# Performance work log

Measured on AMD Instinct MI355X. Metric: run time of the kernel, lower is better.

The kernel has to match this reference:

```python
import jax, jax.numpy as jnp
import numpy as np

# Dimensions (all layers are mLSTM due to the constructor bug: `if w` tests the
# whole truthy `which` list, so signature=(2,1) still yields 3 mLSTM layers).
L, S, B, I = 3, 512, 4, 512      # layers, seq_len, batch, inp_dim
H, D = 8, 64                     # head_num, head_dim
HD = H * D                       # hidden dim = 512
P = 2 * I                        # up_l projection dim (m-branch p_factor = 2)
K = 4                            # causal conv kernel size
EPS = 1e-5
PNAMES = ['ln_g', 'ln_b', 'upl_w', 'upl_b', 'upr_w', 'upr_b', 'conv_w', 'conv_b',
          'wq_w', 'wq_b', 'wk_w', 'wk_b', 'wv_w', 'wv_b', 'wo_w', 'wo_b',
          'wi_w', 'wi_b', 'wf_w', 'wf_b', 'skip_w', 'gn_g', 'gn_b', 'down_w', 'down_b']


def setup_inputs() -> dict:
    key = jax.random.key(0)
    ks = iter(jax.random.split(key, 16))
    def w(shape, fan_in):
        return jax.random.normal(next(ks), shape, jnp.float32) / np.float32(np.sqrt(fan_in))
    return {
        'seq': jax.random.normal(next(ks), (S, B, I), jnp.float32),
        'ln_g': jnp.ones((L, I), jnp.float32), 'ln_b': jnp.zeros((L, I), jnp.float32),
        'upl_w': w((L, P, I), I), 'upl_b': jnp.zeros((L, P), jnp.float32),
        'upr_w': w((L, HD, I), I), 'upr_b': jnp.zeros((L, HD), jnp.float32),
        'conv_w': w((L, K), K), 'conv_b': jnp.zeros((L,), jnp.float32),
        'wq_w': w((L, HD, P), P), 'wq_b': jnp.zeros((L, HD), jnp.float32),
        'wk_w': w((L, HD, P), P), 'wk_b': jnp.zeros((L, HD), jnp.float32),
        'wv_w': w((L, HD, P), P), 'wv_b': jnp.zeros((L, HD), jnp.float32),
        'wo_w': w((L, HD, P), P), 'wo_b': jnp.zeros((L, HD), jnp.float32),
        'wi_w': w((L, H, P), P), 'wi_b': jnp.zeros((L, H), jnp.float32),
        'wf_w': w((L, H, P), P), 'wf_b': jnp.zeros((L, H), jnp.float32),
        'skip_w': w((L, HD, P), P),
        'gn_g': jnp.ones((L, HD), jnp.float32), 'gn_b': jnp.zeros((L, HD), jnp.float32),
        'down_w': w((L, I, HD), HD), 'down_b': jnp.zeros((L, I), jnp.float32),
    }


def _layernorm(x, g, b):
    mu = x.mean(-1, keepdims=True)
    v = ((x - mu) ** 2).mean(-1, keepdims=True)
    return (x - mu) / jnp.sqrt(v + EPS) * g + b


def _groupnorm(x, g, b):
    # GroupNorm(head_num, HD) on (B, HD): normalize each head's D channels
    xh = x.reshape(-1, H, D)
    mu = xh.mean(-1, keepdims=True)
    v = ((xh - mu) ** 2).mean(-1, keepdims=True)
    xn = (xh - mu) / jnp.sqrt(v + EPS)
    return (xn * g.reshape(H, D) + b.reshape(H, D)).reshape(-1, HD)


def _causal_conv(x, w, b):
    # 1-channel causal conv over the feature axis of the per-step vector (B, P)
    xp = jnp.pad(x, ((0, 0), (K - 1, 0)))
    y = b
    for k in range(K):  # K=4, static unroll
        y = y + w[k] * xp[:, k:k + x.shape[1]]
    return y


def _mlstm_step(p, x, state):
    c_, n_, m_ = state
    x_n = _layernorm(x, p['ln_g'], p['ln_b'])
    x_t = x_n @ p['upl_w'].T + p['upl_b']                 # (B, P)
    r_t = x_n @ p['upr_w'].T + p['upr_b']                 # (B, HD)
    x_c = jax.nn.silu(_causal_conv(x_t, p['conv_w'], p['conv_b']))
    q = (x_c @ p['wq_w'].T + p['wq_b']).reshape(-1, H, D)
    k = (x_c @ p['wk_w'].T + p['wk_b']).reshape(-1, H, D) / np.float32(np.sqrt(D))
    v = (x_t @ p['wv_w'].T + p['wv_b']).reshape(-1, H, D)
    i = x_c @ p['wi_w'].T + p['wi_b']                     # (B, H)
    f = x_c @ p['wf_w'].T + p['wf_b']                     # (B, H)
    o = jax.nn.sigmoid(x_t @ p['wo_w'].T + p['wo_b'])     # (B, HD)
    m = jnp.maximum(f + m_, i)                            # stabilizer
    ig = jnp.exp(i - m)
    fg = jnp.exp(f - m + m_)
    c = fg[..., None, None] * c_ + ig[..., None, None] * jnp.einsum('bhd,bhe->bhde', v, k)
    n = fg[..., None] * n_ + ig[..., None] * k
    num = jnp.einsum('bhde,bhe->bhd', c, q)
    den = jnp.maximum(jnp.abs(jnp.einsum('bhd,bhd->bh', n, q)), 1.0)[..., None]
    h = o * (num / den).reshape(-1, HD)
    out = _groupnorm(h, p['gn_g'], p['gn_b']) + x_c @ p['skip_w'].T
    out = out * jax.nn.silu(r_t)
    out = out @ p['down_w'].T + p['down_b']
    return out + x, (c, n, m)


def _forward(seq, params):
    b = seq.shape[1]
    def step(states, x_t):
        new_states = []
        inp = x_t
        for l in range(L):
            pl = {k: v[l] for k, v in params.items()}
            inp, st = _mlstm_step(pl, inp, states[l])
            new_states.append(st)
        return tuple(new_states), inp
    init = tuple((jnp.zeros((b, H, D, D), seq.dtype),
                  jnp.ones((b, H, D), seq.dtype),
                  jnp.zeros((b, H), seq.dtype)) for _ in range(L))
    _, out = jax.lax.scan(step, init, seq)
    return out  # (S, B, I)


def reference(seq, ln_g, ln_b, upl_w, upl_b, upr_w, upr_b, conv_w, conv_b,
              wq_w, wq_b, wk_w, wk_b, wv_w, wv_b, wo_w, wo_b,
              wi_w, wi_b, wf_w, wf_b, skip_w, gn_g, gn_b, down_w, down_b):
    params = dict(zip(PNAMES, [ln_g, ln_b, upl_w, upl_b, upr_w, upr_b, conv_w, conv_b,
                               wq_w, wq_b, wk_w, wk_b, wv_w, wv_b, wo_w, wo_b,
                               wi_w, wi_b, wf_w, wf_b, skip_w, gn_g, gn_b, down_w, down_b]))
    return _forward(seq, params)
```

## Files before the change

### kernel.cpp

```cpp
#include <hip/hip_runtime.h>
#include <hip/hip_bf16.h>
#include <cstdint>
#include <cstddef>

typedef short short8 __attribute__((ext_vector_type(8)));
typedef short short4v __attribute__((ext_vector_type(4)));
typedef float f32x4 __attribute__((ext_vector_type(4)));
typedef __hip_bfloat16 bf16;

#define NROW 2048
#define N1 1536
#define N2 1664
#define N3 1024
#define EPSV 1e-5f

static __device__ __forceinline__ bf16 f2bf(float v){ return __float2bfloat16(v); }
static __device__ __forceinline__ float bfbits2f(short s){
  unsigned u = ((unsigned)(unsigned short)s) << 16;
  float f; __builtin_memcpy(&f, &u, 4); return f;
}
static __device__ __forceinline__ void split_bf(float v, bf16& h, bf16& l){
  h = __float2bfloat16(v);
  l = __float2bfloat16(v - __bfloat162float(h));
}

static __device__ __forceinline__ void gload16(const bf16* g, bf16* l){
  __builtin_amdgcn_global_load_lds(
      (const __attribute__((address_space(1))) void*)(g),
      (__attribute__((address_space(3))) void*)(l), 16, 0, 0);
}

#define MFMA __builtin_amdgcn_mfma_f32_16x16x32_bf16

__global__ __launch_bounds__(256) void pack_w1(const float* __restrict__ upl,
    const float* __restrict__ upr, bf16* __restrict__ dh, bf16* __restrict__ dl)
{
  int l = blockIdx.y, r = blockIdx.x;
  const float* src = (r < 1024) ? upl + ((size_t)l*1024 + r)*512
                                : upr + ((size_t)l*512 + (r-1024))*512;
  size_t o = ((size_t)l*N1 + r)*512;
  for (int c = threadIdx.x; c < 512; c += 256) split_bf(src[c], dh[o+c], dl[o+c]);
}

__global__ __launch_bounds__(256) void pack_w2(const float* __restrict__ wq,
    const float* __restrict__ wk, const float* __restrict__ skp,
    const float* __restrict__ wi, const float* __restrict__ wf,
    bf16* __restrict__ dh, bf16* __restrict__ dl)
{
  int l = blockIdx.y, r = blockIdx.x;
  const float* src; float sc = 1.f;
  if (r < 512)        src = wq  + ((size_t)l*512 + r)*1024;
  else if (r < 1024){ src = wk  + ((size_t)l*512 + r-512)*1024; sc = 0.125f; }
  else if (r < 1536)  src = skp + ((size_t)l*512 + r-1024)*1024;
  else if (r < 1544)  src = wi  + ((size_t)l*8   + r-1536)*1024;
  else if (r < 1552)  src = wf  + ((size_t)l*8   + r-1544)*1024;
  else src = nullptr;
  size_t o = ((size_t)l*N2 + r)*1024;
  for (int c = threadIdx.x; c < 1024; c += 256)
    split_bf(src ? src[c]*sc : 0.f, dh[o+c], dl[o+c]);
}

__global__ __launch_bounds__(256) void pack_w3(const float* __restrict__ wv,
    const float* __restrict__ wo, bf16* __restrict__ dh, bf16* __restrict__ dl)
{
  int l = blockIdx.y, r = blockIdx.x;
  const float* src = (r < 512) ? wv + ((size_t)l*512 + r)*1024
                               : wo + ((size_t)l*512 + (r-512))*1024;
  size_t o = ((size_t)l*N3 + r)*1024;
  for (int c = threadIdx.x; c < 1024; c += 256) split_bf(src[c], dh[o+c], dl[o+c]);
}

__global__ __launch_bounds__(256) void pack_w4(const float* __restrict__ dw,
    bf16* __restrict__ dh, bf16* __restrict__ dl)
{
  int l = blockIdx.y, r = blockIdx.x;
  const float* src = dw + ((size_t)l*512 + r)*512;
  size_t o = ((size_t)l*512 + r)*512;
  for (int c = threadIdx.x; c < 512; c += 256) split_bf(src[c], dh[o+c], dl[o+c]);
}

__global__ __launch_bounds__(256) void pack_bias(
    const float* __restrict__ uplb, const float* __restrict__ uprb,
    const float* __restrict__ wqb,  const float* __restrict__ wkb,
    const float* __restrict__ wib,  const float* __restrict__ wfb,
    const float* __restrict__ wvb,  const float* __restrict__ wob,
    const float* __restrict__ dwb,
    float* __restrict__ b1, float* __restrict__ b2,
    float* __restrict__ b3, float* __restrict__ b4)
{
  int l = blockIdx.x;
  for (int j = threadIdx.x; j < N1; j += 256)
    b1[l*N1+j] = (j < 1024) ? uplb[l*1024+j] : uprb[l*512+j-1024];
  for (int j = threadIdx.x; j < N2; j += 256){
    float v = 0.f;
    if (j < 512)        v = wqb[l*512+j];
    else if (j < 1024)  v = wkb[l*512+j-512]*0.125f;
    else if (j < 1536)  v = 0.f;
    else if (j < 1544)  v = wib[l*8+j-1536];
    else if (j < 1552)  v = wfb[l*8+j-1544];
    b2[l*N2+j] = v;
  }
  for (int j = threadIdx.x; j < N3; j += 256)
    b3[l*N3+j] = (j < 512) ? wvb[l*512+j] : wob[l*512+j-512];
  for (int j = threadIdx.x; j < 512; j += 256)
    b4[l*512+j] = dwb[l*512+j];
}

static __device__ __forceinline__ void gemm_core(
    bf16* __restrict__ sm,
    int bx, int by,
    const bf16* __restrict__ Ah, const bf16* __restrict__ Al,
    const bf16* __restrict__ Wh, const bf16* __restrict__ Wl,
    const float* __restrict__ bias, float* __restrict__ Cf,
    bf16* __restrict__ Cbh, bf16* __restrict__ Cbl,
    const float* __restrict__ resid, int N, int K)
{
  int tid = threadIdx.x;
  int lane = tid & 63, w = tid >> 6;
  int wr = w >> 2, wc = w & 3;
  int m0 = by*128, n0 = bx*128;
  int srow = tid >> 2, sslot = tid & 3;
  int gcol = ((sslot ^ (srow & 3)) * 8);
  const bf16* gAh = Ah + (size_t)(m0 + srow)*K + gcol;
  const bf16* gAl = Al + (size_t)(m0 + srow)*K + gcol;
  const bf16* gBh = Wh + (size_t)(n0 + srow)*K + gcol;
  const bf16* gBl = Wl + (size_t)(n0 + srow)*K + gcol;

  f32x4 acc[4][2];
  for (int i=0;i<4;i++) for (int j=0;j<2;j++) acc[i][j] = (f32x4){0.f,0.f,0.f,0.f};

  int r = lane & 15, g = lane >> 4;
  int xs = (g ^ (r & 3)) * 8;
  int aoff[4], boff[2];
  for (int mi=0;mi<4;mi++) aoff[mi] = (wr*64 + mi*16 + r)*32 + xs;
  for (int ni=0;ni<2;ni++) boff[ni] = (wc*32 + ni*16 + r)*32 + xs;

  int nt = K >> 5;
#define STAGE_T(base, kk) do{ bf16* _d = sm + (base) + tid*8; \
    gload16(gAh + (kk), _d); \
    gload16(gAl + (kk), _d + 4096); \
    gload16(gBh + (kk), _d + 8192); \
    gload16(gBl + (kk), _d + 12288); }while(0)

  STAGE_T(0, 0);
  asm volatile("s_waitcnt vmcnt(0)" ::: "memory");
  __builtin_amdgcn_s_barrier();

  for (int t = 0; t < nt; ++t){
    int cb = (t & 1) * 16384;
    if (t + 1 < nt) STAGE_T(16384 - cb, (t+1)*32);
    const bf16* sA = sm + cb;
    short8 ah[4], al[4], bh2[2], bl2[2];
    for (int mi=0;mi<4;mi++){
      ah[mi] = *(const short8*)(sA + aoff[mi]);
      al[mi] = *(const short8*)(sA + 4096 + aoff[mi]);
    }
    for (int ni=0;ni<2;ni++){
      bh2[ni] = *(const short8*)(sA + 8192 + boff[ni]);
      bl2[ni] = *(const short8*)(sA + 12288 + boff[ni]);
    }
    for (int mi=0;mi<4;mi++) for (int ni=0;ni<2;ni++)
      acc[mi][ni] = MFMA(ah[mi], bh2[ni], acc[mi][ni],0,0,0);
    for (int mi=0;mi<4;mi++) for (int ni=0;ni<2;ni++)
      acc[mi][ni] = MFMA(al[mi], bh2[ni], acc[mi][ni],0,0,0);
    for (int mi=0;mi<4;mi++) for (int ni=0;ni<2;ni++)
      acc[mi][ni] = MFMA(ah[mi], bl2[ni], acc[mi][ni],0,0,0);
    asm volatile("s_waitcnt vmcnt(0)" ::: "memory");
    __builtin_amdgcn_s_barrier();
  }
#undef STAGE_T

  for (int mi=0;mi<4;mi++) for (int ni=0;ni<2;ni++){
    int col = n0 + wc*32 + ni*16 + r;
    float bv = bias ? bias[col] : 0.f;
    for (int j=0;j<4;j++){
      int row = m0 + wr*64 + mi*16 + g*4 + j;
      float v = acc[mi][ni][j] + bv;
      size_t o = (size_t)row*N + col;
      if (resid) v += resid[o];
      if (Cf) Cf[o] = v;
      if (Cbh) split_bf(v, Cbh[o], Cbl[o]);
    }
  }
}

__global__ __launch_bounds__(512) void gemm_std(
    const bf16* __restrict__ Ah, const bf16* __restrict__ Al,
    const bf16* __restrict__ Wh, const bf16* __restrict__ Wl,
    const float* __restrict__ bias, float* __restrict__ Cf,
    bf16* __restrict__ Cbh, bf16* __restrict__ Cbl,
    const float* __restrict__ resid, int N, int K, int nbx)
{
  __shared__ bf16 sm[2*4*4096];
  int id = blockIdx.x;
  int cpx = gridDim.x >> 3;
  int swz = (id & 7)*cpx + (id >> 3);
  int by = swz / nbx, bx = swz - by*nbx;
  gemm_core(sm, bx, by, Ah, Al, Wh, Wl, bias, Cf, Cbh, Cbl, resid, N, K);
}

__global__ __launch_bounds__(512) void gemm23(
    const bf16* __restrict__ A2h, const bf16* __restrict__ A2l,
    const bf16* __restrict__ W2h, const bf16* __restrict__ W2l,
    const float* __restrict__ b2,
    bf16* __restrict__ c2h, bf16* __restrict__ c2l,
    const bf16* __restrict__ A3h, const bf16* __restrict__ A3l,
    const bf16* __restrict__ W3h, const bf16* __restrict__ W3l,
    const float* __restrict__ b3,
    bf16* __restrict__ c3h, bf16* __restrict__ c3l)
{
  __shared__ bf16 sm[2*4*4096];
  int id = blockIdx.x;
  int cpx = gridDim.x >> 3;
  int swz = (id & 7)*cpx + (id >> 3);
  int by = swz / 21, bx = swz - by*21;
  if (bx < 13)
    gemm_core(sm, bx, by, A2h, A2l, W2h, W2l, b2, nullptr, c2h, c2l, nullptr, N2, 1024);
  else
    gemm_core(sm, bx-13, by, A3h, A3l, W3h, W3l, b3, nullptr, c3h, c3l, nullptr, N3, 1024);
}

__global__ __launch_bounds__(256) void ln_kernel(const float* __restrict__ x,
    const float* __restrict__ g, const float* __restrict__ bt,
    bf16* __restrict__ xnh, bf16* __restrict__ xnl)
{
  int row = blockIdx.x, t = threadIdx.x;
  float v0 = x[(size_t)row*512 + t], v1 = x[(size_t)row*512 + 256 + t];
  float s = v0 + v1, ss = v0*v0 + v1*v1;
  for (int m=1; m<64; m<<=1){ s += __shfl_xor(s,m); ss += __shfl_xor(ss,m); }
  __shared__ float sh[8];
  int w = t >> 6, lane = t & 63;
  if (lane == 0){ sh[w] = s; sh[4+w] = ss; }
  __syncthreads();
  s = sh[0]+sh[1]+sh[2]+sh[3]; ss = sh[4]+sh[5]+sh[6]+sh[7];
  float mu = s*(1.f/512.f), var = ss*(1.f/512.f) - mu*mu;
  float rs = rsqrtf(var + EPSV);
  float y0 = (v0-mu)*rs*g[t]     + bt[t];
  float y1 = (v1-mu)*rs*g[256+t] + bt[256+t];
  split_bf(y0, xnh[(size_t)row*512 + t],       xnl[(size_t)row*512 + t]);
  split_bf(y1, xnh[(size_t)row*512 + 256 + t], xnl[(size_t)row*512 + 256 + t]);
}

__global__ __launch_bounds__(256) void conv_kernel(
    const bf16* __restrict__ c1h, const bf16* __restrict__ c1l,
    const float* __restrict__ cw, const float* __restrict__ cb,
    bf16* __restrict__ xch, bf16* __restrict__ xcl,
    bf16* __restrict__ xth, bf16* __restrict__ xtl)
{
  int row = blockIdx.x;
  size_t rb = (size_t)row*N1;
  float w0=cw[0], w1=cw[1], w2=cw[2], w3=cw[3], bb=cb[0];
  int j0 = threadIdx.x*4;
  float x[7];
  for (int k=0;k<3;k++){
    int j = j0-3+k;
    x[k] = (j>=0) ? (bfbits2f(*(const short*)(c1h+rb+j)) +
                     bfbits2f(*(const short*)(c1l+rb+j))) : 0.f;
  }
  short4v h4 = *(const short4v*)(c1h+rb+j0);
  short4v l4 = *(const short4v*)(c1l+rb+j0);
  for (int k=0;k<4;k++) x[3+k] = bfbits2f(h4[k]) + bfbits2f(l4[k]);
  for (int i=0;i<4;i++){
    float y = bb + w0*x[i] + w1*x[i+1] + w2*x[i+2] + w3*x[i+3];
    float sg = 1.f/(1.f + __expf(-y));
    size_t o = (size_t)row*1024 + j0 + i;
    split_bf(y*sg, xch[o], xcl[o]);
    split_bf(x[3+i], xth[o], xtl[o]);
  }
}

__global__ __launch_bounds__(512) void scan_kernel(
    const bf16* __restrict__ c2h, const bf16* __restrict__ c2l,
    float* __restrict__ rowterm, float* __restrict__ colterm,
    float* __restrict__ den0)
{
  int bh = blockIdx.x, b = bh >> 3, h = bh & 7;
  int t = threadIdx.x;
  size_t rowoff = (size_t)(t*4+b)*N2;
  float fv = bfbits2f(*(const short*)(c2h+rowoff+1544+h)) +
             bfbits2f(*(const short*)(c2l+rowoff+1544+h));
  float iv = bfbits2f(*(const short*)(c2h+rowoff+1536+h)) +
             bfbits2f(*(const short*)(c2l+rowoff+1536+h));
  __shared__ double a[512];
  a[t] = (double)fv; __syncthreads();
  for (int off=1; off<512; off<<=1){
    double x = a[t];
    double y = (t >= off) ? a[t-off] : 0.0;
    __syncthreads();
    a[t] = x + y;
    __syncthreads();
  }
  float ct = (float)((double)iv - a[t]);
  colterm[bh*512 + t] = ct;
  __shared__ float mx[512];
  mx[t] = ct; __syncthreads();
  for (int off=1; off<512; off<<=1){
    float x = mx[t];
    float y = (t >= off) ? mx[t-off] : -3.0e38f;
    __syncthreads();
    mx[t] = fmaxf(x, y);
    __syncthreads();
  }
  float rt = -fmaxf(0.f, mx[t]);
  rowterm[bh*512 + t] = rt;
  float qs = 0.f;
  size_t qoff = rowoff + h*64;
  for (int c8=0;c8<8;c8++){
    short8 hx = *(const short8*)(c2h+qoff+c8*8);
    short8 lx = *(const short8*)(c2l+qoff+c8*8);
    for (int e=0;e<8;e++) qs += bfbits2f(hx[e]) + bfbits2f(lx[e]);
  }
  den0[bh*512 + t] = __expf(rt) * qs;
}

__global__ __launch_bounds__(512) void vtrans_kernel(
    const bf16* __restrict__ c3h, const bf16* __restrict__ c3l,
    bf16* __restrict__ vTh, bf16* __restrict__ vTl)
{
  int bh = blockIdx.y, b = bh >> 3, h = bh & 7;
  int d0 = blockIdx.x*8;
  int s = threadIdx.x;
  for (int dd=0; dd<8; dd++){
    int d = d0 + dd;
    size_t i = (size_t)(s*4+b)*N3 + h*64 + d;
    size_t o = ((size_t)bh*64 + d)*512 + s;
    vTh[o] = c3h[i];
    vTl[o] = c3l[i];
  }
}

__global__ __launch_bounds__(256) void attn_kernel(
    const bf16* __restrict__ c2h, const bf16* __restrict__ c2l,
    const bf16* __restrict__ vTh, const bf16* __restrict__ vTl,
    const float* __restrict__ rowt, const float* __restrict__ colt,
    float* __restrict__ num, float* __restrict__ denp)
{
  __shared__ bf16 Ph[32*64], Pl[32*64];
  int lane = threadIdx.x & 63, w = threadIdx.x >> 6;
  int tb = blockIdx.x, bh = blockIdx.y, b = bh >> 3, h = bh & 7;
  int t0 = tb*32;
  int r = lane & 15, g = lane >> 4;
  int rq = g*4;

  short8 qh[2][2], ql[2][2];
  for (int mi=0;mi<2;mi++) for (int k0=0;k0<2;k0++){
    size_t off = (size_t)((t0+mi*16+r)*4+b)*N2 + h*64 + k0*32 + g*8;
    qh[mi][k0] = *(const short8*)(c2h+off);
    ql[mi][k0] = *(const short8*)(c2l+off);
  }
  const float* rt = rowt + bh*512;
  const float* ctm = colt + bh*512;
  float rtv[2][4];
  for (int mi=0;mi<2;mi++) for (int j=0;j<4;j++) rtv[mi][j] = rt[t0+mi*16+rq+j];

  f32x4 accPV[2];
  for (int i=0;i<2;i++) accPV[i] = (f32x4){0.f,0.f,0.f,0.f};
  float rsum[2][4];
  for (int i=0;i<2;i++) for (int j=0;j<4;j++) rsum[i][j] = 0.f;

  int nsb = (tb >> 1) + 1;
  for (int sb=0; sb<nsb; ++sb){
    int s0 = sb*64;
    f32x4 acc[2];
    for (int i=0;i<2;i++) acc[i] = (f32x4){0.f,0.f,0.f,0.f};
    short8 kh[2], kl[2];
    for (int k0=0;k0<2;k0++){
      size_t off = (size_t)((s0+w*16+r)*4+b)*N2 + 512 + h*64 + k0*32 + g*8;
      kh[k0] = *(const short8*)(c2h+off);
      kl[k0] = *(const short8*)(c2l+off);
    }
    for (int k0=0;k0<2;k0++){
      for (int mi=0;mi<2;mi++) acc[mi] = MFMA(qh[mi][k0], kh[k0], acc[mi],0,0,0);
      for (int mi=0;mi<2;mi++) acc[mi] = MFMA(ql[mi][k0], kh[k0], acc[mi],0,0,0);
      for (int mi=0;mi<2;mi++) acc[mi] = MFMA(qh[mi][k0], kl[k0], acc[mi],0,0,0);
    }
    int sl = w*16 + r;
    int s = s0 + sl;
    float ctv = ctm[s];
    for (int mi=0;mi<2;mi++){
      for (int j=0;j<4;j++){
        int tloc = mi*16 + rq + j;
        int t = t0 + tloc;
        float wg = (s <= t) ? __expf(rtv[mi][j] + ctv) : 0.f;
        float gv = acc[mi][j] * wg;
        rsum[mi][j] += gv;
        int col = ((((sl>>3) ^ (tloc&7))<<3) | (sl&7));
        split_bf(gv, Ph[tloc*64+col], Pl[tloc*64+col]);
      }
    }
    __syncthreads();
    short8 vh[2], vl[2];
    for (int k0=0;k0<2;k0++){
      size_t off = ((size_t)bh*64 + w*16 + r)*512 + s0 + k0*32 + g*8;
      vh[k0] = *(const short8*)(vTh+off);
      vl[k0] = *(const short8*)(vTl+off);
    }
    for (int k0=0;k0<2;k0++){
      short8 ph[2], pl[2];
      for (int mi=0;mi<2;mi++){
        int tloc = mi*16 + r;
        int slot = (k0*4 + g) ^ (tloc&7);
        ph[mi] = *(const short8*)(&Ph[tloc*64 + slot*8]);
        pl[mi] = *(const short8*)(&Pl[tloc*64 + slot*8]);
      }
      for (int mi=0;mi<2;mi++) accPV[mi] = MFMA(ph[mi], vh[k0], accPV[mi],0,0,0);
      for (int mi=0;mi<2;mi++) accPV[mi] = MFMA(pl[mi], vh[k0], accPV[mi],0,0,0);
      for (int mi=0;mi<2;mi++) accPV[mi] = MFMA(ph[mi], vl[k0], accPV[mi],0,0,0);
    }
    __syncthreads();
  }

  for (int mi=0;mi<2;mi++)
    for (int j=0;j<4;j++){
      int t = t0 + mi*16 + rq + j;
      num[((size_t)bh*512 + t)*64 + w*16 + r] = accPV[mi][j];
    }
  for (int mi=0;mi<2;mi++)
    for (int j=0;j<4;j++){
      float v = rsum[mi][j];
      v += __shfl_xor(v,1); v += __shfl_xor(v,2);
      v += __shfl_xor(v,4); v += __shfl_xor(v,8);
      if (r == 0){
        int t = t0 + mi*16 + rq + j;
        denp[((size_t)bh*512 + t)*4 + w] = v;
      }
    }
}

__global__ __launch_bounds__(512) void h_kernel(
    const float* __restrict__ num, const float* __restrict__ den0,
    const float* __restrict__ denp,
    const bf16* __restrict__ c2h, const bf16* __restrict__ c2l,
    const bf16* __restrict__ c3h, const bf16* __restrict__ c3l,
    const bf16* __restrict__ c1h, const bf16* __restrict__ c1l,
    const float* __restrict__ gng, const float* __restrict__ gnb,
    bf16* __restrict__ oph, bf16* __restrict__ opl)
{
  int row = blockIdx.x, t = row >> 2, b = row & 3;
  int h = threadIdx.x >> 6, d = threadIdx.x & 63;
  int bh = b*8 + h;
  size_t bt = (size_t)bh*512 + t;
  float dn = den0[bt];
  for (int p=0; p<4; p++) dn += denp[bt*4 + p];
  dn = fmaxf(fabsf(dn), 1.f);
  float nv = num[bt*64 + d];
  size_t io = (size_t)row*N3 + 512 + h*64 + d;
  float ov = bfbits2f(*(const short*)(c3h+io)) + bfbits2f(*(const short*)(c3l+io));
  float o = 1.f/(1.f + __expf(-ov));
  float hv = o * nv / dn;
  float s = hv, ss = hv*hv;
  for (int m=1; m<64; m<<=1){ s += __shfl_xor(s,m); ss += __shfl_xor(ss,m); }
  float mu = s*(1.f/64.f), var = ss*(1.f/64.f) - mu*mu;
  float gn = (hv - mu)*rsqrtf(var + EPSV)*gng[h*64+d] + gnb[h*64+d];
  size_t ks = (size_t)row*N2 + 1024 + h*64 + d;
  float sk = bfbits2f(*(const short*)(c2h+ks)) + bfbits2f(*(const short*)(c2l+ks));
  size_t kr = (size_t)row*N1 + 1024 + h*64 + d;
  float rv = bfbits2f(*(const short*)(c1h+kr)) + bfbits2f(*(const short*)(c1l+kr));
  float y = (gn + sk) * (rv/(1.f + __expf(-rv)));
  size_t oo = (size_t)row*512 + h*64 + d;
  split_bf(y, oph[oo], opl[oo]);
}

extern "C" void kernel_launch(void* const* d_in, const int* in_sizes, int n_in,
                              void* d_out, int out_size, void* d_ws, size_t ws_size,
                              hipStream_t stream)
{
  (void)in_sizes; (void)n_in; (void)out_size; (void)ws_size;
  const float* seq    = (const float*)d_in[0];
  const float* ln_g   = (const float*)d_in[1];
  const float* ln_b   = (const float*)d_in[2];
  const float* upl_w  = (const float*)d_in[3];
  const float* upl_b  = (const float*)d_in[4];
  const float* upr_w  = (const float*)d_in[5];
  const float* upr_b  = (const float*)d_in[6];
  const float* conv_w = (const float*)d_in[7];
  const float* conv_b = (const float*)d_in[8];
  const float* wq_w   = (const float*)d_in[9];
  const float* wq_b   = (const float*)d_in[10];
  const float* wk_w   = (const float*)d_in[11];
  const float* wk_b   = (const float*)d_in[12];
  const float* wv_w   = (const float*)d_in[13];
  const float* wv_b   = (const float*)d_in[14];
  const float* wo_w   = (const float*)d_in[15];
  const float* wo_b   = (const float*)d_in[16];
  const float* wi_w   = (const float*)d_in[17];
  const float* wi_b   = (const float*)d_in[18];
  const float* wf_w   = (const float*)d_in[19];
  const float* wf_b   = (const float*)d_in[20];
  const float* skip_w = (const float*)d_in[21];
  const float* gn_g   = (const float*)d_in[22];
  const float* gn_b   = (const float*)d_in[23];
  const float* down_w = (const float*)d_in[24];
  const float* down_b = (const float*)d_in[25];

  char* ws = (char*)d_ws;
  size_t off = 0;
  auto alloc = [&](size_t bytes)->char*{
    char* p = ws + off; off = (off + bytes + 255) & ~(size_t)255; return p;
  };
  bf16*  W1h = (bf16*)alloc((size_t)3*N1*512*2);
  bf16*  W1l = (bf16*)alloc((size_t)3*N1*512*2);
  bf16*  W2h = (bf16*)alloc((size_t)3*N2*1024*2);
  bf16*  W2l = (bf16*)alloc((size_t)3*N2*1024*2);
  bf16*  W3h = (bf16*)alloc((size_t)3*N3*1024*2);
  bf16*  W3l = (bf16*)alloc((size_t)3*N3*1024*2);
  bf16*  W4h = (bf16*)alloc((size_t)3*512*512*2);
  bf16*  W4l = (bf16*)alloc((size_t)3*512*512*2);
  float* b1  = (float*)alloc((size_t)3*N1*4);
  float* b2  = (float*)alloc((size_t)3*N2*4);
  float* b3  = (float*)alloc((size_t)3*N3*4);
  float* b4  = (float*)alloc((size_t)3*512*4);
  bf16*  xnh = (bf16*)alloc((size_t)NROW*512*2);
  bf16*  xnl = (bf16*)alloc((size_t)NROW*512*2);
  bf16*  c1h = (bf16*)alloc((size_t)NROW*N1*2);
  bf16*  c1l = (bf16*)alloc((size_t)NROW*N1*2);
  bf16*  xth = (bf16*)alloc((size_t)NROW*1024*2);
  bf16*  xtl = (bf16*)alloc((size_t)NROW*1024*2);
  bf16*  xch = (bf16*)alloc((size_t)NROW*1024*2);
  bf16*  xcl = (bf16*)alloc((size_t)NROW*1024*2);
  bf16*  c2h = (bf16*)alloc((size_t)NROW*N2*2);
  bf16*  c2l = (bf16*)alloc((size_t)NROW*N2*2);
  bf16*  c3h = (bf16*)alloc((size_t)NROW*N3*2);
  bf16*  c3l = (bf16*)alloc((size_t)NROW*N3*2);
  bf16*  vTh = (bf16*)alloc((size_t)32*64*512*2);
  bf16*  vTl = (bf16*)alloc((size_t)32*64*512*2);
  float* rowt= (float*)alloc((size_t)32*512*4);
  float* colt= (float*)alloc((size_t)32*512*4);
  float* den0= (float*)alloc((size_t)32*512*4);
  float* denp= (float*)alloc((size_t)32*512*4*4);
  float* num = (float*)alloc((size_t)32*512*64*4);
  bf16*  oph = (bf16*)alloc((size_t)NROW*512*2);
  bf16*  opl = (bf16*)alloc((size_t)NROW*512*2);
  float* xA  = (float*)alloc((size_t)NROW*512*4);
  float* xB  = (float*)alloc((size_t)NROW*512*4);

  pack_w1<<<dim3(N1,3), 256, 0, stream>>>(upl_w, upr_w, W1h, W1l);
  pack_w2<<<dim3(N2,3), 256, 0, stream>>>(wq_w, wk_w, skip_w, wi_w, wf_w, W2h, W2l);
  pack_w3<<<dim3(N3,3), 256, 0, stream>>>(wv_w, wo_w, W3h, W3l);
  pack_w4<<<dim3(512,3), 256, 0, stream>>>(down_w, W4h, W4l);
  pack_bias<<<3, 256, 0, stream>>>(upl_b, upr_b, wq_b, wk_b, wi_b, wf_b,
                                   wv_b, wo_b, down_b, b1, b2, b3, b4);

  for (int l = 0; l < 3; l++){
    const float* x_in = (l == 0) ? seq : ((l == 1) ? xA : xB);
    float* x_out = (l == 0) ? xA : ((l == 1) ? xB : (float*)d_out);

    ln_kernel<<<NROW, 256, 0, stream>>>(x_in, ln_g + l*512, ln_b + l*512, xnh, xnl);
    gemm_std<<<12*16, 512, 0, stream>>>(
        xnh, xnl, W1h + (size_t)l*N1*512, W1l + (size_t)l*N1*512,
        b1 + l*N1, nullptr, c1h, c1l, nullptr, N1, 512, 12);
    conv_kernel<<<NROW, 256, 0, stream>>>(c1h, c1l, conv_w + l*4, conv_b + l,
                                          xch, xcl, xth, xtl);
    gemm23<<<21*16, 512, 0, stream>>>(
        xch, xcl, W2h + (size_t)l*N2*1024, W2l + (size_t)l*N2*1024, b2 + l*N2,
        c2h, c2l,
        xth, xtl, W3h + (size_t)l*N3*1024, W3l + (size_t)l*N3*1024, b3 + l*N3,
        c3h, c3l);
    scan_kernel<<<32, 512, 0, stream>>>(c2h, c2l, rowt, colt, den0);
    vtrans_kernel<<<dim3(8,32), 512, 0, stream>>>(c3h, c3l, vTh, vTl);
    attn_kernel<<<dim3(16,32), 256, 0, stream>>>(c2h, c2l, vTh, vTl,
                                                 rowt, colt, num, denp);
    h_kernel<<<NROW, 512, 0, stream>>>(num, den0, denp, c2h, c2l, c3h, c3l,
                                       c1h, c1l, gn_g + l*512, gn_b + l*512,
                                       oph, opl);
    gemm_std<<<4*16, 512, 0, stream>>>(
        oph, opl, W4h + (size_t)l*512*512, W4l + (size_t)l*512*512,
        b4 + l*512, x_out, nullptr, nullptr, x_in, 512, 512, 4);
  }
}
```

Measured before the change: 459.8 us.

## Use 32x32 MFMA GEMM tiles, wave-level scan, and move den0 into h_kernel

After: 502.3 us. 9.2% more time.

```diff
diff --git a/kernel.cpp b/kernel.cpp
--- a/kernel.cpp
+++ b/kernel.cpp
@@ -6,6 +6,7 @@
 typedef short short8 __attribute__((ext_vector_type(8)));
 typedef short short4v __attribute__((ext_vector_type(4)));
 typedef float f32x4 __attribute__((ext_vector_type(4)));
+typedef float f32x16 __attribute__((ext_vector_type(16)));
 typedef __hip_bfloat16 bf16;
 
 #define NROW 2048
@@ -30,7 +31,10 @@
       (__attribute__((address_space(3))) void*)(l), 16, 0, 0);
 }
 
-#define MFMA __builtin_amdgcn_mfma_f32_16x16x32_bf16
+#define MFMA   __builtin_amdgcn_mfma_f32_16x16x32_bf16
+#define MFMA32 __builtin_amdgcn_mfma_f32_32x32x16_bf16
+
+static __device__ __forceinline__ int fsw(int row){ return (row ^ (row >> 2)) & 3; }
 
 __global__ __launch_bounds__(256) void pack_w1(const float* __restrict__ upl,
     const float* __restrict__ upr, bf16* __restrict__ dh, bf16* __restrict__ dl)
@@ -117,30 +121,42 @@
 {
   int tid = threadIdx.x;
   int lane = tid & 63, w = tid >> 6;
-  int wr = w >> 2, wc = w & 3;
+  int wr = w >> 1, wc = w & 1;
   int m0 = by*128, n0 = bx*128;
   int srow = tid >> 2, sslot = tid & 3;
-  int gcol = ((sslot ^ (srow & 3)) * 8);
+  int gcol = (sslot ^ fsw(srow)) * 8;
   const bf16* gAh = Ah + (size_t)(m0 + srow)*K + gcol;
   const bf16* gAl = Al + (size_t)(m0 + srow)*K + gcol;
   const bf16* gBh = Wh + (size_t)(n0 + srow)*K + gcol;
   const bf16* gBl = Wl + (size_t)(n0 + srow)*K + gcol;
-
-  f32x4 acc[4][2];
-  for (int i=0;i<4;i++) for (int j=0;j<2;j++) acc[i][j] = (f32x4){0.f,0.f,0.f,0.f};
-
-  int r = lane & 15, g = lane >> 4;
-  int xs = (g ^ (r & 3)) * 8;
-  int aoff[4], boff[2];
-  for (int mi=0;mi<4;mi++) aoff[mi] = (wr*64 + mi*16 + r)*32 + xs;
-  for (int ni=0;ni<2;ni++) boff[ni] = (wc*32 + ni*16 + r)*32 + xs;
+  size_t pstr = (size_t)64*K;
+
+  f32x16 acc[2][2];
+  #pragma unroll
+  for (int i=0;i<2;i++)
+    #pragma unroll
+    for (int j=0;j<2;j++)
+      #pragma unroll
+      for (int q=0;q<16;q++) acc[i][j][q] = 0.f;
+
+  int l31 = lane & 31, l5 = lane >> 5;
+  int aoff[2][2], boff[2][2];
+  #pragma unroll
+  for (int mi=0;mi<2;mi++)
+    #pragma unroll
+    for (int kh=0;kh<2;kh++){
+      int ra = wr*64 + mi*32 + l31;
+      aoff[mi][kh] = ra*32 + ((kh*2 + l5) ^ fsw(ra))*8;
+      int rb = wc*64 + mi*32 + l31;
+      boff[mi][kh] = rb*32 + ((kh*2 + l5) ^ fsw(rb))*8;
+    }
 
   int nt = K >> 5;
 #define STAGE_T(base, kk) do{ bf16* _d = sm + (base) + tid*8; \
-    gload16(gAh + (kk), _d); \
-    gload16(gAl + (kk), _d + 4096); \
-    gload16(gBh + (kk), _d + 8192); \
-    gload16(gBl + (kk), _d + 12288); }while(0)
+    gload16(gAh + (kk), _d);          gload16(gAh + (kk) + pstr, _d + 2048); \
+    gload16(gAl + (kk), _d + 4096);   gload16(gAl + (kk) + pstr, _d + 6144); \
+    gload16(gBh + (kk), _d + 8192);   gload16(gBh + (kk) + pstr, _d + 10240); \
+    gload16(gBl + (kk), _d + 12288);  gload16(gBl + (kk) + pstr, _d + 14336); }while(0)
 
   STAGE_T(0, 0);
   asm volatile("s_waitcnt vmcnt(0)" ::: "memory");
@@ -150,41 +166,58 @@
     int cb = (t & 1) * 16384;
     if (t + 1 < nt) STAGE_T(16384 - cb, (t+1)*32);
     const bf16* sA = sm + cb;
-    short8 ah[4], al[4], bh2[2], bl2[2];
-    for (int mi=0;mi<4;mi++){
-      ah[mi] = *(const short8*)(sA + aoff[mi]);
-      al[mi] = *(const short8*)(sA + 4096 + aoff[mi]);
-    }
-    for (int ni=0;ni<2;ni++){
-      bh2[ni] = *(const short8*)(sA + 8192 + boff[ni]);
-      bl2[ni] = *(const short8*)(sA + 12288 + boff[ni]);
-    }
-    for (int mi=0;mi<4;mi++) for (int ni=0;ni<2;ni++)
-      acc[mi][ni] = MFMA(ah[mi], bh2[ni], acc[mi][ni],0,0,0);
-    for (int mi=0;mi<4;mi++) for (int ni=0;ni<2;ni++)
-      acc[mi][ni] = MFMA(al[mi], bh2[ni], acc[mi][ni],0,0,0);
-    for (int mi=0;mi<4;mi++) for (int ni=0;ni<2;ni++)
-      acc[mi][ni] = MFMA(ah[mi], bl2[ni], acc[mi][ni],0,0,0);
+    short8 ah[2][2], al[2][2], bh2[2][2], bl2[2][2];
+    #pragma unroll
+    for (int mi=0;mi<2;mi++)
+      #pragma unroll
+      for (int kh=0;kh<2;kh++){
+        ah[mi][kh]  = *(const short8*)(sA + aoff[mi][kh]);
+        al[mi][kh]  = *(const short8*)(sA + 4096 + aoff[mi][kh]);
+        bh2[mi][kh] = *(const short8*)(sA + 8192 + boff[mi][kh]);
+        bl2[mi][kh] = *(const short8*)(sA + 12288 + boff[mi][kh]);
+      }
+    #pragma unroll
+    for (int kh=0;kh<2;kh++){
+      #pragma unroll
+      for (int mi=0;mi<2;mi++)
+        #pragma unroll
+        for (int ni=0;ni<2;ni++)
+          acc[mi][ni] = MFMA32(ah[mi][kh], bh2[ni][kh], acc[mi][ni],0,0,0);
+      #pragma unroll
+      for (int mi=0;mi<2;mi++)
+        #pragma unroll
+        for (int ni=0;ni<2;ni++)
+          acc[mi][ni] = MFMA32(al[mi][kh], bh2[ni][kh], acc[mi][ni],0,0,0);
+      #pragma unroll
+      for (int mi=0;mi<2;mi++)
+        #pragma unroll
+        for (int ni=0;ni<2;ni++)
+          acc[mi][ni] = MFMA32(ah[mi][kh], bl2[ni][kh], acc[mi][ni],0,0,0);
+    }
     asm volatile("s_waitcnt vmcnt(0)" ::: "memory");
     __builtin_amdgcn_s_barrier();
   }
 #undef STAGE_T
 
-  for (int mi=0;mi<4;mi++) for (int ni=0;ni<2;ni++){
-    int col = n0 + wc*32 + ni*16 + r;
-    float bv = bias ? bias[col] : 0.f;
-    for (int j=0;j<4;j++){
-      int row = m0 + wr*64 + mi*16 + g*4 + j;
-      float v = acc[mi][ni][j] + bv;
-      size_t o = (size_t)row*N + col;
-      if (resid) v += resid[o];
-      if (Cf) Cf[o] = v;
-      if (Cbh) split_bf(v, Cbh[o], Cbl[o]);
-    }
-  }
-}
-
-__global__ __launch_bounds__(512) void gemm_std(
+  #pragma unroll
+  for (int mi=0;mi<2;mi++)
+    #pragma unroll
+    for (int ni=0;ni<2;ni++){
+      int col = n0 + wc*64 + ni*32 + l31;
+      float bv = bias ? bias[col] : 0.f;
+      #pragma unroll
+      for (int q=0;q<16;q++){
+        int row = m0 + wr*64 + mi*32 + (q&3) + 8*(q>>2) + 4*l5;
+        float v = acc[mi][ni][q] + bv;
+        size_t o = (size_t)row*N + col;
+        if (resid) v += resid[o];
+        if (Cf) Cf[o] = v;
+        if (Cbh) split_bf(v, Cbh[o], Cbl[o]);
+      }
+    }
+}
+
+__global__ __launch_bounds__(256) void gemm_std(
     const bf16* __restrict__ Ah, const bf16* __restrict__ Al,
     const bf16* __restrict__ Wh, const bf16* __restrict__ Wl,
     const float* __restrict__ bias, float* __restrict__ Cf,
@@ -199,7 +232,7 @@
   gemm_core(sm, bx, by, Ah, Al, Wh, Wl, bias, Cf, Cbh, Cbl, resid, N, K);
 }
 
-__global__ __launch_bounds__(512) void gemm23(
+__global__ __launch_bounds__(256) void gemm23(
     const bf16* __restrict__ A2h, const bf16* __restrict__ A2l,
     const bf16* __restrict__ W2h, const bf16* __restrict__ W2l,
     const float* __restrict__ b2,
@@ -269,48 +302,47 @@
   }
 }
 
-__global__ __launch_bounds__(512) void scan_kernel(
+__global__ __launch_bounds__(64) void scan_kernel(
     const bf16* __restrict__ c2h, const bf16* __restrict__ c2l,
-    float* __restrict__ rowterm, float* __restrict__ colterm,
-    float* __restrict__ den0)
+    float* __restrict__ rowterm, float* __restrict__ colterm)
 {
   int bh = blockIdx.x, b = bh >> 3, h = bh & 7;
-  int t = threadIdx.x;
-  size_t rowoff = (size_t)(t*4+b)*N2;
-  float fv = bfbits2f(*(const short*)(c2h+rowoff+1544+h)) +
-             bfbits2f(*(const short*)(c2l+rowoff+1544+h));
-  float iv = bfbits2f(*(const short*)(c2h+rowoff+1536+h)) +
-             bfbits2f(*(const short*)(c2l+rowoff+1536+h));
-  __shared__ double a[512];
-  a[t] = (double)fv; __syncthreads();
-  for (int off=1; off<512; off<<=1){
-    double x = a[t];
-    double y = (t >= off) ? a[t-off] : 0.0;
-    __syncthreads();
-    a[t] = x + y;
-    __syncthreads();
-  }
-  float ct = (float)((double)iv - a[t]);
-  colterm[bh*512 + t] = ct;
-  __shared__ float mx[512];
-  mx[t] = ct; __syncthreads();
-  for (int off=1; off<512; off<<=1){
-    float x = mx[t];
-    float y = (t >= off) ? mx[t-off] : -3.0e38f;
-    __syncthreads();
-    mx[t] = fmaxf(x, y);
-    __syncthreads();
-  }
-  float rt = -fmaxf(0.f, mx[t]);
-  rowterm[bh*512 + t] = rt;
-  float qs = 0.f;
-  size_t qoff = rowoff + h*64;
-  for (int c8=0;c8<8;c8++){
-    short8 hx = *(const short8*)(c2h+qoff+c8*8);
-    short8 lx = *(const short8*)(c2l+qoff+c8*8);
-    for (int e=0;e<8;e++) qs += bfbits2f(hx[e]) + bfbits2f(lx[e]);
-  }
-  den0[bh*512 + t] = __expf(rt) * qs;
+  int lane = threadIdx.x;
+  double fv[8]; float iv[8];
+  for (int j=0;j<8;j++){
+    int t = lane*8 + j;
+    size_t ro = (size_t)(t*4+b)*N2;
+    fv[j] = (double)(bfbits2f(*(const short*)(c2h+ro+1544+h)) +
+                     bfbits2f(*(const short*)(c2l+ro+1544+h)));
+    iv[j] = bfbits2f(*(const short*)(c2h+ro+1536+h)) +
+            bfbits2f(*(const short*)(c2l+ro+1536+h));
+  }
+  double ps[8]; double s = 0.0;
+  for (int j=0;j<8;j++){ s += fv[j]; ps[j] = s; }
+  double run = s;
+  for (int o=1;o<64;o<<=1){
+    double u = __shfl_up(run, o);
+    if (lane >= o) run += u;
+  }
+  double excl = run - s;
+  float ct[8];
+  for (int j=0;j<8;j++){
+    ct[j] = (float)((double)iv[j] - (excl + ps[j]));
+    colterm[bh*512 + lane*8 + j] = ct[j];
+  }
+  float pm[8]; float mm = -3.0e38f;
+  for (int j=0;j<8;j++){ mm = fmaxf(mm, ct[j]); pm[j] = mm; }
+  float incl = mm;
+  for (int o=1;o<64;o<<=1){
+    float u = __shfl_up(incl, o);
+    if (lane >= o) incl = fmaxf(incl, u);
+  }
+  float ex = __shfl_up(incl, 1);
+  if (lane == 0) ex = -3.0e38f;
+  for (int j=0;j<8;j++){
+    float inc = fmaxf(ex, pm[j]);
+    rowterm[bh*512 + lane*8 + j] = -fmaxf(0.f, inc);
+  }
 }
 
 __global__ __launch_bounds__(512) void vtrans_kernel(
@@ -428,8 +460,8 @@
 }
 
 __global__ __launch_bounds__(512) void h_kernel(
-    const float* __restrict__ num, const float* __restrict__ den0,
-    const float* __restrict__ denp,
+    const float* __restrict__ num, const float* __restrict__ denp,
+    const float* __restrict__ rowt,
     const bf16* __restrict__ c2h, const bf16* __restrict__ c2l,
     const bf16* __restrict__ c3h, const bf16* __restrict__ c3l,
     const bf16* __restrict__ c1h, const bf16* __restrict__ c1l,
@@ -440,7 +472,10 @@
   int h = threadIdx.x >> 6, d = threadIdx.x & 63;
   int bh = b*8 + h;
   size_t bt = (size_t)bh*512 + t;
-  float dn = den0[bt];
+  size_t qo = (size_t)row*N2 + h*64 + d;
+  float qs = bfbits2f(*(const short*)(c2h+qo)) + bfbits2f(*(const short*)(c2l+qo));
+  for (int m=1; m<64; m<<=1) qs += __shfl_xor(qs, m);
+  float dn = __expf(rowt[bt]) * qs;
   for (int p=0; p<4; p++) dn += denp[bt*4 + p];
   dn = fmaxf(fabsf(dn), 1.f);
   float nv = num[bt*64 + d];
@@ -526,7 +561,6 @@
   bf16*  vTl = (bf16*)alloc((size_t)32*64*512*2);
   float* rowt= (float*)alloc((size_t)32*512*4);
   float* colt= (float*)alloc((size_t)32*512*4);
-  float* den0= (float*)alloc((size_t)32*512*4);
   float* denp= (float*)alloc((size_t)32*512*4*4);
   float* num = (float*)alloc((size_t)32*512*64*4);
   bf16*  oph = (bf16*)alloc((size_t)NROW*512*2);
@@ -546,24 +580,24 @@
     float* x_out = (l == 0) ? xA : ((l == 1) ? xB : (float*)d_out);
 
     ln_kernel<<<NROW, 256, 0, stream>>>(x_in, ln_g + l*512, ln_b + l*512, xnh, xnl);
-    gemm_std<<<12*16, 512, 0, stream>>>(
+    gemm_std<<<12*16, 256, 0, stream>>>(
         xnh, xnl, W1h + (size_t)l*N1*512, W1l + (size_t)l*N1*512,
         b1 + l*N1, nullptr, c1h, c1l, nullptr, N1, 512, 12);
     conv_kernel<<<NROW, 256, 0, stream>>>(c1h, c1l, conv_w + l*4, conv_b + l,
                                           xch, xcl, xth, xtl);
-    gemm23<<<21*16, 512, 0, stream>>>(
+    gemm23<<<21*16, 256, 0, stream>>>(
         xch, xcl, W2h + (size_t)l*N2*1024, W2l + (size_t)l*N2*1024, b2 + l*N2,
         c2h, c2l,
         xth, xtl, W3h + (size_t)l*N3*1024, W3l + (size_t)l*N3*1024, b3 + l*N3,
         c3h, c3l);
-    scan_kernel<<<32, 512, 0, stream>>>(c2h, c2l, rowt, colt, den0);
+    scan_kernel<<<32, 64, 0, stream>>>(c2h, c2l, rowt, colt);
     vtrans_kernel<<<dim3(8,32), 512, 0, stream>>>(c3h, c3l, vTh, vTl);
     attn_kernel<<<dim3(16,32), 256, 0, stream>>>(c2h, c2l, vTh, vTl,
                                                  rowt, colt, num, denp);
-    h_kernel<<<NROW, 512, 0, stream>>>(num, den0, denp, c2h, c2l, c3h, c3l,
+    h_kernel<<<NROW, 512, 0, stream>>>(num, denp, rowt, c2h, c2l, c3h, c3l,
                                        c1h, c1l, gn_g + l*512, gn_b + l*512,
                                        oph, opl);
-    gemm_std<<<4*16, 512, 0, stream>>>(
+    gemm_std<<<4*16, 256, 0, stream>>>(
         oph, opl, W4h + (size_t)l*512*512, W4l + (size_t)l*512*512,
         b4 + l*512, x_out, nullptr, nullptr, x_in, 512, 512, 4);
   }
```
